# Optimization experiments

Measured on AMD Instinct MI355X. Metric: run time of the kernel, lower is better.

## Reference

```python
import jax, jax.numpy as jnp
import numpy as np

DECAY = 0.8
EPS = 1e-5
H, C, D = 1, 4096, 512   # num_codebooks, codebook_size, dim
B, N = 8, 4096           # batch, tokens


def l2norm(t):
    return t / jnp.clip(jnp.linalg.norm(t, axis=-1, keepdims=True), 1e-12, None)


def setup_inputs() -> dict:
    key = jax.random.key(0)
    k1, k2, k3 = jax.random.split(key, 3)
    x = jax.random.normal(k1, (B, N, D), jnp.float32)
    embed = l2norm(jax.random.normal(k2, (H, C, D), jnp.float32))  # codebook rows are unit-norm
    cluster_size = jax.random.uniform(k3, (H, C), jnp.float32) * 10.0
    embed_avg = embed * cluster_size[..., None]
    return {"x": x, "embed": embed, "cluster_size": cluster_size, "embed_avg": embed_avg}


def reference(x, embed, cluster_size, embed_avg):
    # pack: 'h * d' with h = 1 codebook
    flatten = x.reshape(H, B * N, D)
    # cosine-sim distances (inputs assumed pre-l2norm'd by wrapper; embed is unit-norm)
    dist = jnp.einsum('hnd,hcd->hnc', flatten, embed)          # (h, n, c)
    # gumbel_sample with temperature 0 / eval == argmax
    embed_ind = jnp.argmax(dist, axis=-1)                      # (h, n)
    onehot = jax.nn.one_hot(embed_ind, C, dtype=flatten.dtype) # (h, n, c)
    # training-path quantize via one-hot matmul
    quantize = jnp.einsum('hnc,hcd->hnd', onehot, embed).reshape(B, N, D)
    # EMA codebook update
    bins = onehot.sum(axis=1)                                  # (h, c)
    new_cluster = cluster_size * DECAY + bins * (1.0 - DECAY)
    embed_sum = jnp.einsum('hnd,hnc->hcd', flatten, onehot)    # (h, c, d)
    new_embed_avg = embed_avg * DECAY + embed_sum * (1.0 - DECAY)
    tot = new_cluster.sum(axis=-1, keepdims=True)
    smoothed = (new_cluster + EPS) / (tot + C * EPS) * tot     # laplace_smoothing * total
    new_embed = l2norm(new_embed_avg / smoothed[..., None])
    return (quantize,
            embed_ind.reshape(B, N),
            dist.reshape(B, N, C),
            new_cluster,
            new_embed_avg,
            new_embed)
```

## Files before the change

### kernel.cpp

```cpp
#include <hip/hip_runtime.h>
#include <hip/hip_fp16.h>
#include <cstdint>
#include <cstddef>

#define CB    4096
#define DD    512
#define M_TOK 32768
#define DECAY_F 0.8f
#define OMD_F   0.2f
#define EPS_F   1e-5f

#define OFF_QUANT ((size_t)0)
#define SZ_QUANT  ((size_t)M_TOK * DD)
#define OFF_IND   (OFF_QUANT + SZ_QUANT)
#define SZ_IND    ((size_t)M_TOK)
#define OFF_DIST  (OFF_IND + SZ_IND)
#define SZ_DIST   ((size_t)M_TOK * CB)
#define OFF_NC    (OFF_DIST + SZ_DIST)
#define SZ_NC     ((size_t)CB)
#define OFF_AVG   (OFF_NC + SZ_NC)
#define SZ_AVG    ((size_t)CB * DD)
#define OFF_NEMB  (OFF_AVG + SZ_AVG)

typedef unsigned short ushort_b;
typedef __attribute__((ext_vector_type(8))) short f16x8;
typedef __attribute__((ext_vector_type(4))) float f32x4;

__global__ __launch_bounds__(256) void k_init(int* __restrict__ bins,
                                              float* __restrict__ tot) {
  int id = blockIdx.x * 256 + threadIdx.x;
  if (id < CB) bins[id] = 0;
  if (id == 0) *tot = 0.0f;
}

__global__ __launch_bounds__(256) void k_split(const float* __restrict__ src,
                                               ushort_b* __restrict__ hi,
                                               ushort_b* __restrict__ lo) {
  size_t id = (size_t)blockIdx.x * 256 + threadIdx.x;
  const float* p = src + id * 8;
  float4 v0 = *(const float4*)p;
  float4 v1 = *(const float4*)(p + 4);
  float f[8] = {v0.x, v0.y, v0.z, v0.w, v1.x, v1.y, v1.z, v1.w};
  ushort_b h[8], l[8];
#pragma unroll
  for (int j = 0; j < 8; ++j) {
    __half hh = __float2half(f[j]);
    h[j] = __half_as_ushort(hh);
    float r = f[j] - __half2float(hh);
    l[j] = __half_as_ushort(__float2half(r));
  }
  uint4 H, L;
  H.x = h[0] | ((unsigned)h[1] << 16); H.y = h[2] | ((unsigned)h[3] << 16);
  H.z = h[4] | ((unsigned)h[5] << 16); H.w = h[6] | ((unsigned)h[7] << 16);
  L.x = l[0] | ((unsigned)l[1] << 16); L.y = l[2] | ((unsigned)l[3] << 16);
  L.z = l[4] | ((unsigned)l[5] << 16); L.w = l[6] | ((unsigned)l[7] << 16);
  *(uint4*)(hi + id * 8) = H;
  *(uint4*)(lo + id * 8) = L;
}

#define TSZ 4096

__device__ __forceinline__ void gload16(const void* g, void* l) {
  __builtin_amdgcn_global_load_lds((const __attribute__((address_space(1))) unsigned int*)g,
                                   (__attribute__((address_space(3))) unsigned int*)l,
                                   16, 0, 0);
}

__global__ __launch_bounds__(256) void k_dist_mfma(const ushort_b* __restrict__ Xhi,
                                                   const ushort_b* __restrict__ Xlo,
                                                   const ushort_b* __restrict__ Ehi,
                                                   const ushort_b* __restrict__ Elo,
                                                   float* __restrict__ dist) {
  __shared__ __align__(16) ushort_b lds[4 * TSZ];
  const int tid  = threadIdx.x;
  const int lane = tid & 63;
  const int wid  = tid >> 6;
  const int wr   = wid >> 1;
  const int wc   = wid & 1;
  const int bn   = blockIdx.x;
  const int bm   = blockIdx.y;

  const size_t abase = (size_t)bm * 128 * DD;
  const size_t bbase = (size_t)bn * 128 * DD;

  const int chunk0 = tid;
  const int chunk1 = tid + 256;
  const int row0 = chunk0 >> 2, slot0 = chunk0 & 3;
  const int row1 = chunk1 >> 2, slot1 = chunk1 & 3;
  const int q0 = slot0 ^ ((row0 >> 1) & 3);
  const int q1 = slot1 ^ ((row1 >> 1) & 3);
  const size_t g0 = (size_t)row0 * DD + q0 * 8;
  const size_t g1 = (size_t)row1 * DD + q1 * 8;
  const int lb0 = (wid * 64) * 8;
  const int lb1 = (wid * 64 + 256) * 8;

  f32x4 acc[4][4];
#pragma unroll
  for (int i = 0; i < 4; ++i)
#pragma unroll
    for (int j = 0; j < 4; ++j) acc[i][j] = (f32x4){0.f, 0.f, 0.f, 0.f};

  const int qr = lane >> 4;
  int aoff[4], boff[4];
#pragma unroll
  for (int mi = 0; mi < 4; ++mi) {
    int row = wr * 64 + mi * 16 + (lane & 15);
    aoff[mi] = row * 32 + ((qr ^ ((row >> 1) & 3)) << 3);
  }
#pragma unroll
  for (int ni = 0; ni < 4; ++ni) {
    int col = wc * 64 + ni * 16 + (lane & 15);
    boff[ni] = col * 32 + ((qr ^ ((col >> 1) & 3)) << 3);
  }

  for (int kt = 0; kt < DD; kt += 32) {
    gload16(Xhi + abase + g0 + kt, &lds[0 * TSZ + lb0]);
    gload16(Xhi + abase + g1 + kt, &lds[0 * TSZ + lb1]);
    gload16(Xlo + abase + g0 + kt, &lds[1 * TSZ + lb0]);
    gload16(Xlo + abase + g1 + kt, &lds[1 * TSZ + lb1]);
    gload16(Ehi + bbase + g0 + kt, &lds[2 * TSZ + lb0]);
    gload16(Ehi + bbase + g1 + kt, &lds[2 * TSZ + lb1]);
    gload16(Elo + bbase + g0 + kt, &lds[3 * TSZ + lb0]);
    gload16(Elo + bbase + g1 + kt, &lds[3 * TSZ + lb1]);
    __syncthreads();

    f16x8 ah[4], al[4], bh[4], bl[4];
#pragma unroll
    for (int mi = 0; mi < 4; ++mi) {
      ah[mi] = *(const f16x8*)&lds[0 * TSZ + aoff[mi]];
      al[mi] = *(const f16x8*)&lds[1 * TSZ + aoff[mi]];
    }
#pragma unroll
    for (int ni = 0; ni < 4; ++ni) {
      bh[ni] = *(const f16x8*)&lds[2 * TSZ + boff[ni]];
      bl[ni] = *(const f16x8*)&lds[3 * TSZ + boff[ni]];
    }
#pragma unroll
    for (int mi = 0; mi < 4; ++mi)
#pragma unroll
      for (int ni = 0; ni < 4; ++ni) {
        acc[mi][ni] = __builtin_amdgcn_mfma_f32_16x16x32_f16(ah[mi], bh[ni], acc[mi][ni], 0, 0, 0);
        acc[mi][ni] = __builtin_amdgcn_mfma_f32_16x16x32_f16(al[mi], bh[ni], acc[mi][ni], 0, 0, 0);
        acc[mi][ni] = __builtin_amdgcn_mfma_f32_16x16x32_f16(ah[mi], bl[ni], acc[mi][ni], 0, 0, 0);
      }
    __syncthreads();
  }

  const int rbase = bm * 128 + wr * 64 + (lane >> 4) * 4;
  const int cbase = bn * 128 + wc * 64 + (lane & 15);
#pragma unroll
  for (int mi = 0; mi < 4; ++mi)
#pragma unroll
    for (int r = 0; r < 4; ++r) {
      float* drow = dist + (size_t)(rbase + mi * 16 + r) * CB + cbase;
#pragma unroll
      for (int ni = 0; ni < 4; ++ni) drow[ni * 16] = acc[mi][ni][r];
    }
}

__global__ __launch_bounds__(256) void k_argmax(const float* __restrict__ dist,
                                                float* __restrict__ ind_f,
                                                int* __restrict__ idx_ws,
                                                int* __restrict__ bins) {
  const int row = blockIdx.x;
  const float* p = dist + (size_t)row * CB;
  const int tid = threadIdx.x;
  float best = -3.402823466e38f;
  int bi = 0;
#pragma unroll
  for (int it = 0; it < 4; ++it) {
    int j4 = (tid + it * 256) << 2;
    float4 v = *(const float4*)(p + j4);
    if (v.x > best) { best = v.x; bi = j4; }
    if (v.y > best) { best = v.y; bi = j4 + 1; }
    if (v.z > best) { best = v.z; bi = j4 + 2; }
    if (v.w > best) { best = v.w; bi = j4 + 3; }
  }
  for (int off = 32; off; off >>= 1) {
    float ov = __shfl_down(best, off);
    int   oi = __shfl_down(bi, off);
    if (ov > best || (ov == best && oi < bi)) { best = ov; bi = oi; }
  }
  __shared__ float sv[4];
  __shared__ int   si[4];
  int wid = tid >> 6;
  if ((tid & 63) == 0) { sv[wid] = best; si[wid] = bi; }
  __syncthreads();
  if (tid == 0) {
#pragma unroll
    for (int w = 1; w < 4; ++w)
      if (sv[w] > best || (sv[w] == best && si[w] < bi)) { best = sv[w]; bi = si[w]; }
    ind_f[row]  = (float)bi;
    idx_ws[row] = bi;
    atomicAdd(&bins[bi], 1);
  }
}

__global__ __launch_bounds__(256) void k_scan(const int* __restrict__ bins,
                                              int* __restrict__ cursor) {
  const int tid  = threadIdx.x;
  const int lane = tid & 63;
  const int wid  = tid >> 6;
  int v[16];
  const int base = tid * 16;
  int run = 0;
#pragma unroll
  for (int i = 0; i < 16; ++i) { int t = bins[base + i]; v[i] = run; run += t; }
  int x = run;
  for (int d = 1; d < 64; d <<= 1) {
    int y = __shfl_up(x, d);
    if (lane >= d) x += y;
  }
  __shared__ int wtot[4];
  if (lane == 63) wtot[wid] = x;
  __syncthreads();
  int woff = 0;
  for (int w = 0; w < wid; ++w) woff += wtot[w];
  int ex = woff + x - run;
#pragma unroll
  for (int i = 0; i < 16; ++i) cursor[base + i] = ex + v[i];
}

__global__ __launch_bounds__(256) void k_scatter_ids(const int* __restrict__ idx_ws,
                                                     int* __restrict__ cursor,
                                                     int* __restrict__ tlist) {
  int n = blockIdx.x * 256 + threadIdx.x;
  int c = idx_ws[n];
  int slot = atomicAdd(&cursor[c], 1);
  tlist[slot] = n;
}

__global__ __launch_bounds__(128) void k_embed_sum(const float* __restrict__ X,
                                                   const float* __restrict__ E,
                                                   const float* __restrict__ eavg,
                                                   const int* __restrict__ cursor,
                                                   const int* __restrict__ bins,
                                                   const int* __restrict__ tlist,
                                                   float* __restrict__ quant,
                                                   float* __restrict__ avg) {
  const int c   = blockIdx.x;
  const int tid = threadIdx.x;
  const int d4  = tid * 4;
  const int end = cursor[c];
  const int cnt = bins[c];
  const int start = end - cnt;
  float4 e = *(const float4*)(E + (size_t)c * DD + d4);
  float4 s = {0.f, 0.f, 0.f, 0.f};
  for (int t = start; t < end; ++t) {
    int n = tlist[t];
    float4 xv = *(const float4*)(X + (size_t)n * DD + d4);
    s.x += xv.x; s.y += xv.y; s.z += xv.z; s.w += xv.w;
    *(float4*)(quant + (size_t)n * DD + d4) = e;
  }
  float4 ea = *(const float4*)(eavg + (size_t)c * DD + d4);
  float4 o;
  o.x = DECAY_F * ea.x + OMD_F * s.x;
  o.y = DECAY_F * ea.y + OMD_F * s.y;
  o.z = DECAY_F * ea.z + OMD_F * s.z;
  o.w = DECAY_F * ea.w + OMD_F * s.w;
  *(float4*)(avg + (size_t)c * DD + d4) = o;
}

__global__ __launch_bounds__(256) void k_cluster(const float* __restrict__ cs,
                                                 const int* __restrict__ bins,
                                                 float* __restrict__ nc_out,
                                                 float* __restrict__ tot) {
  int c = blockIdx.x * 256 + threadIdx.x;
  float nc = DECAY_F * cs[c] + OMD_F * (float)bins[c];
  nc_out[c] = nc;
  float s = nc;
  for (int off = 32; off; off >>= 1) s += __shfl_down(s, off);
  if ((threadIdx.x & 63) == 0) atomicAdd(tot, s);
}

__global__ __launch_bounds__(128) void k_norm(const float* __restrict__ avg,
                                              const float* __restrict__ nc,
                                              const float* __restrict__ tot,
                                              float* __restrict__ out) {
  int c = blockIdx.x;
  int tid = threadIdx.x;
  const float* row = avg + (size_t)c * DD;
  float4 v = *(const float4*)(row + tid * 4);
  float ss = v.x * v.x + v.y * v.y + v.z * v.z + v.w * v.w;
  for (int off = 32; off; off >>= 1) ss += __shfl_down(ss, off);
  __shared__ float s2[2];
  if ((tid & 63) == 0) s2[tid >> 6] = ss;
  __syncthreads();
  float sumsq = s2[0] + s2[1];
  float t = *tot;
  float sm = (nc[c] + EPS_F) / (t + (float)CB * EPS_F) * t;
  float nrm = sqrtf(sumsq) / sm;
  float denom = fmaxf(nrm, 1e-12f);
  float scale = 1.0f / (sm * denom);
  float4 o;
  o.x = v.x * scale; o.y = v.y * scale; o.z = v.z * scale; o.w = v.w * scale;
  *(float4*)(out + (size_t)c * DD + tid * 4) = o;
}

extern "C" void kernel_launch(void* const* d_in, const int* in_sizes, int n_in,
                              void* d_out, int out_size, void* d_ws, size_t ws_size,
                              hipStream_t stream) {
  const float* x     = (const float*)d_in[0];
  const float* embed = (const float*)d_in[1];
  const float* cs    = (const float*)d_in[2];
  const float* eavg  = (const float*)d_in[3];

  float* out    = (float*)d_out;
  float* quant  = out + OFF_QUANT;
  float* indf   = out + OFF_IND;
  float* dist   = out + OFF_DIST;
  float* ncout  = out + OFF_NC;
  float* avgout = out + OFF_AVG;
  float* nemb   = out + OFF_NEMB;

  int*   idx_ws = (int*)d_ws;
  int*   bins   = idx_ws + M_TOK;
  float* tot    = (float*)(bins + CB);

  ushort_b* xhi = (ushort_b*)quant;
  ushort_b* xlo = xhi + (size_t)M_TOK * DD;
  ushort_b* ehi = (ushort_b*)nemb;
  ushort_b* elo = ehi + (size_t)CB * DD;

  int* tlist  = (int*)nemb;
  int* cursor = tlist + M_TOK;

  k_init<<<dim3(16), dim3(256), 0, stream>>>(bins, tot);
  k_split<<<dim3(M_TOK * DD / 8 / 256), dim3(256), 0, stream>>>(x, xhi, xlo);
  k_split<<<dim3(CB * DD / 8 / 256), dim3(256), 0, stream>>>(embed, ehi, elo);
  k_dist_mfma<<<dim3(CB / 128, M_TOK / 128), dim3(256), 0, stream>>>(xhi, xlo, ehi, elo, dist);
  k_argmax<<<dim3(M_TOK), dim3(256), 0, stream>>>(dist, indf, idx_ws, bins);
  k_scan<<<dim3(1), dim3(256), 0, stream>>>(bins, cursor);
  k_scatter_ids<<<dim3(M_TOK / 256), dim3(256), 0, stream>>>(idx_ws, cursor, tlist);
  k_embed_sum<<<dim3(CB), dim3(128), 0, stream>>>(x, embed, eavg, cursor, bins, tlist, quant, avgout);
  k_cluster<<<dim3(16), dim3(256), 0, stream>>>(cs, bins, ncout, tot);
  k_norm<<<dim3(CB), dim3(128), 0, stream>>>(avgout, ncout, tot, nemb);
}
```

Before: 1.111 ms.

## Fuse argmax into distance GEMM epilogue via packed 64-bit atomicMax keys

The separate argmax kernel, which re-read the full 32768x4096 fp32 distance matrix, is replaced by a per-tile argmax in the MFMA GEMM epilogue. Each tile reduces its row maximum with shuffles and merges it globally through a 64-bit atomicMax on an order-preserving float encoding packed with the inverted column index, so ties resolve to the lowest index. A small finalize kernel decodes the keys and builds the bins. This removes a 512 MB read of the distance matrix, at the cost of 32 atomics per row and a scratch key buffer placed in the embed_avg output region, which is overwritten later.

```diff
diff --git a/kernel.cpp b/kernel.cpp
--- a/kernel.cpp
+++ b/kernel.cpp
@@ -23,12 +23,15 @@
 #define OFF_NEMB  (OFF_AVG + SZ_AVG)
 
 typedef unsigned short ushort_b;
+typedef unsigned long long u64;
 typedef __attribute__((ext_vector_type(8))) short f16x8;
 typedef __attribute__((ext_vector_type(4))) float f32x4;
 
-__global__ __launch_bounds__(256) void k_init(int* __restrict__ bins,
+__global__ __launch_bounds__(256) void k_init(u64* __restrict__ keys,
+                                              int* __restrict__ bins,
                                               float* __restrict__ tot) {
   int id = blockIdx.x * 256 + threadIdx.x;
+  keys[id] = 0ull;
   if (id < CB) bins[id] = 0;
   if (id == 0) *tot = 0.0f;
 }
@@ -70,7 +73,8 @@
                                                    const ushort_b* __restrict__ Xlo,
                                                    const ushort_b* __restrict__ Ehi,
                                                    const ushort_b* __restrict__ Elo,
-                                                   float* __restrict__ dist) {
+                                                   float* __restrict__ dist,
+                                                   u64* __restrict__ keys) {
   __shared__ __align__(16) ushort_b lds[4 * TSZ];
   const int tid  = threadIdx.x;
   const int lane = tid & 63;
@@ -153,47 +157,37 @@
 #pragma unroll
     for (int r = 0; r < 4; ++r) {
       float* drow = dist + (size_t)(rbase + mi * 16 + r) * CB + cbase;
-#pragma unroll
-      for (int ni = 0; ni < 4; ++ni) drow[ni * 16] = acc[mi][ni][r];
+      float best = acc[mi][0][r];
+      int   bc   = cbase;
+      drow[0] = best;
+#pragma unroll
+      for (int ni = 1; ni < 4; ++ni) {
+        float v = acc[mi][ni][r];
+        drow[ni * 16] = v;
+        if (v > best) { best = v; bc = cbase + ni * 16; }
+      }
+      unsigned ub  = __float_as_uint(best);
+      unsigned enc = (ub & 0x80000000u) ? ~ub : (ub | 0x80000000u);
+      u64 key = ((u64)enc << 32) | (u64)(0xFFFFFFFFu - (unsigned)bc);
+#pragma unroll
+      for (int m = 8; m; m >>= 1) {
+        u64 ok = __shfl_xor(key, m);
+        if (ok > key) key = ok;
+      }
+      if ((lane & 15) == 0) atomicMax(&keys[rbase + mi * 16 + r], key);
     }
 }
 
-__global__ __launch_bounds__(256) void k_argmax(const float* __restrict__ dist,
-                                                float* __restrict__ ind_f,
-                                                int* __restrict__ idx_ws,
-                                                int* __restrict__ bins) {
-  const int row = blockIdx.x;
-  const float* p = dist + (size_t)row * CB;
-  const int tid = threadIdx.x;
-  float best = -3.402823466e38f;
-  int bi = 0;
-#pragma unroll
-  for (int it = 0; it < 4; ++it) {
-    int j4 = (tid + it * 256) << 2;
-    float4 v = *(const float4*)(p + j4);
-    if (v.x > best) { best = v.x; bi = j4; }
-    if (v.y > best) { best = v.y; bi = j4 + 1; }
-    if (v.z > best) { best = v.z; bi = j4 + 2; }
-    if (v.w > best) { best = v.w; bi = j4 + 3; }
-  }
-  for (int off = 32; off; off >>= 1) {
-    float ov = __shfl_down(best, off);
-    int   oi = __shfl_down(bi, off);
-    if (ov > best || (ov == best && oi < bi)) { best = ov; bi = oi; }
-  }
-  __shared__ float sv[4];
-  __shared__ int   si[4];
-  int wid = tid >> 6;
-  if ((tid & 63) == 0) { sv[wid] = best; si[wid] = bi; }
-  __syncthreads();
-  if (tid == 0) {
-#pragma unroll
-    for (int w = 1; w < 4; ++w)
-      if (sv[w] > best || (sv[w] == best && si[w] < bi)) { best = sv[w]; bi = si[w]; }
-    ind_f[row]  = (float)bi;
-    idx_ws[row] = bi;
-    atomicAdd(&bins[bi], 1);
-  }
+__global__ __launch_bounds__(256) void k_finalize(const u64* __restrict__ keys,
+                                                  float* __restrict__ ind_f,
+                                                  int* __restrict__ idx_ws,
+                                                  int* __restrict__ bins) {
+  int row = blockIdx.x * 256 + threadIdx.x;
+  u64 key = keys[row];
+  int col = (int)(0xFFFFFFFFu - (unsigned)(key & 0xFFFFFFFFull));
+  ind_f[row]  = (float)col;
+  idx_ws[row] = col;
+  atomicAdd(&bins[col], 1);
 }
 
 __global__ __launch_bounds__(256) void k_scan(const int* __restrict__ bins,
@@ -322,14 +316,16 @@
   ushort_b* ehi = (ushort_b*)nemb;
   ushort_b* elo = ehi + (size_t)CB * DD;
 
+  u64* keys = (u64*)avgout;
+
   int* tlist  = (int*)nemb;
   int* cursor = tlist + M_TOK;
 
-  k_init<<<dim3(16), dim3(256), 0, stream>>>(bins, tot);
+  k_init<<<dim3(128), dim3(256), 0, stream>>>(keys, bins, tot);
   k_split<<<dim3(M_TOK * DD / 8 / 256), dim3(256), 0, stream>>>(x, xhi, xlo);
   k_split<<<dim3(CB * DD / 8 / 256), dim3(256), 0, stream>>>(embed, ehi, elo);
-  k_dist_mfma<<<dim3(CB / 128, M_TOK / 128), dim3(256), 0, stream>>>(xhi, xlo, ehi, elo, dist);
-  k_argmax<<<dim3(M_TOK), dim3(256), 0, stream>>>(dist, indf, idx_ws, bins);
+  k_dist_mfma<<<dim3(CB / 128, M_TOK / 128), dim3(256), 0, stream>>>(xhi, xlo, ehi, elo, dist, keys);
+  k_finalize<<<dim3(128), dim3(256), 0, stream>>>(keys, indf, idx_ws, bins);
   k_scan<<<dim3(1), dim3(256), 0, stream>>>(bins, cursor);
   k_scatter_ids<<<dim3(M_TOK / 256), dim3(256), 0, stream>>>(idx_ws, cursor, tlist);
   k_embed_sum<<<dim3(CB), dim3(128), 0, stream>>>(x, embed, eavg, cursor, bins, tlist, quant, avgout);
```

Measured after the change: 1.123 ms. No clear change (+1.1%).
